# Kernel tuning notes

Measured on AMD Instinct MI355X. Metric: run time of the kernel, lower is better.

Reference implementation:

```python
import jax, jax.numpy as jnp
import numpy as np
import math

D_MODEL = 1024
RPN_D = 256
SUP_HW = 20  # support feature map is 20x20 -> 400 tokens


def _positional_encoding(max_len, d_model):
    pos = np.arange(max_len, dtype=np.float32)[:, None]
    div = np.exp(np.arange(0, d_model, 2, dtype=np.float32) * -(math.log(10000.0) / float(d_model)))
    pe = np.zeros((max_len, d_model), dtype=np.float32)
    pe[:, 0::2] = np.sin(pos * div)
    pe[:, 1::2] = np.cos(pos * div)
    return jnp.asarray(pe)


def setup_inputs() -> dict:
    key = jax.random.key(0)
    ks = jax.random.split(key, 6)
    B, S, H = 4, 5, 4
    fh, fw = 64, 64
    base_feat = jax.random.normal(ks[0], (B, D_MODEL, fh, fw), dtype=jnp.float32)
    support_feat = jax.random.normal(ks[1], (B, S, D_MODEL, SUP_HW, SUP_HW), dtype=jnp.float32)
    Qw = jax.random.normal(ks[2], (H, RPN_D, D_MODEL), dtype=jnp.float32) * 0.01
    Qb = jnp.zeros((H, RPN_D), dtype=jnp.float32)
    Kw = jax.random.normal(ks[3], (H, RPN_D, D_MODEL), dtype=jnp.float32) * 0.01
    Kb = jnp.zeros((H, RPN_D), dtype=jnp.float32)
    Mw = jax.random.normal(ks[4], (D_MODEL, H * D_MODEL), dtype=jnp.float32) * 0.02
    Mb = jnp.zeros((D_MODEL,), dtype=jnp.float32)
    return {"base_feat": base_feat, "support_feat": support_feat,
            "Qw": Qw, "Qb": Qb, "Kw": Kw, "Kb": Kb, "Mw": Mw, "Mb": Mb}


def reference(base_feat, support_feat, Qw, Qb, Kw, Kb, Mw, Mb):
    B, C, fh, fw = base_feat.shape
    S = support_feat.shape[1]
    H = Qw.shape[0]
    Lq = fh * fw
    Lk = SUP_HW * SUP_HW

    # support_mat: [S, B, Lk, C]  (transpose(0,1) then flatten spatial, then transpose)
    support_mat = jnp.transpose(support_feat, (1, 0, 2, 3, 4)).reshape(S, B, C, Lk)
    support_mat = jnp.transpose(support_mat, (0, 1, 3, 2))
    # query_mat: [B, Lq, C]
    query_mat = jnp.transpose(base_feat.reshape(B, C, Lq), (0, 2, 1))

    pe = _positional_encoding(400, D_MODEL)[:Lk]  # [Lk, C]
    s_mat = support_mat + pe[None, None]          # [S, B, Lk, C]

    # per-head projections (q is independent of shot, compute once)
    q = jnp.einsum('blc,hdc->hbld', query_mat, Qw) + Qb[:, None, None, :]   # [H,B,Lq,d]
    k = jnp.einsum('sbkc,hdc->hsbkd', s_mat, Kw) + Kb[:, None, None, None, :]  # [H,S,B,Lk,d]

    scores = jnp.einsum('hbld,hsbkd->hsblk', q, k) / math.sqrt(RPN_D)  # [H,S,B,Lq,Lk]
    attn = jax.nn.softmax(scores, axis=-1)
    z = jnp.einsum('hsblk,sbkc->hsblc', attn, s_mat)  # [H,S,B,Lq,C]

    # shot_mode == 'mean'
    z = jnp.mean(z, axis=1)  # [H,B,Lq,C]

    # concat heads along feature dim (head order preserved): [B,Lq,H*C]
    att = jnp.transpose(z, (1, 2, 0, 3)).reshape(B, Lq, H * C)
    att = jax.nn.relu(att @ Mw.T + Mb)  # [B,Lq,C]

    att = jnp.transpose(att, (0, 2, 1)).reshape(B, C, fh, fw)
    # attention_type == 'product'
    correlation_feat = base_feat * att
    return correlation_feat
```

## Files before the change

kernel.cpp:

```cpp
#include <hip/hip_runtime.h>
#include <stdint.h>

#define DEVI __device__ __forceinline__

typedef __attribute__((ext_vector_type(8))) short bf16x8;
typedef __attribute__((ext_vector_type(4))) float f32x4;
typedef __attribute__((ext_vector_type(4))) unsigned short us4;
typedef unsigned short u16;

constexpr int B_ = 4, S_ = 5, H_ = 4, C_ = 1024, D_ = 256;
constexpr int LQ = 4096, LK = 400, LKP = 448;

DEVI u16 f2b(float f){
  uint32_t x = __float_as_uint(f);
  uint32_t r = (x + 0x7FFFu + ((x >> 16) & 1u)) >> 16;
  return (u16)r;
}

typedef __attribute__((address_space(1))) const void ASG;
typedef __attribute__((address_space(3))) void ASL;
DEVI void gload16(const void* g, void* l){
  __builtin_amdgcn_global_load_lds((ASG*)g, (ASL*)l, 16, 0, 0);
}

__global__ __launch_bounds__(256) void k_cvt(const float* __restrict__ s, u16* __restrict__ d, int n4){
  int i = blockIdx.x*256 + threadIdx.x;
  if (i >= n4) return;
  float4 v = ((const float4*)s)[i];
  us4 o; o.x = f2b(v.x); o.y = f2b(v.y); o.z = f2b(v.z); o.w = f2b(v.w);
  *(us4*)(d + (size_t)i*4) = o;
}

__global__ __launch_bounds__(256) void k_transpose_x(const float* __restrict__ base, u16* __restrict__ Xb){
  __shared__ float t[32][33];
  int l0 = blockIdx.x*32, c0 = blockIdx.y*32, b = blockIdx.z;
  int tx = threadIdx.x & 31, ty = threadIdx.x >> 5;
  const float* src = base + ((size_t)b*C_ + c0)*LQ + l0;
  #pragma unroll
  for (int i=0;i<4;i++){ int cc = ty + i*8; t[cc][tx] = src[(size_t)cc*LQ + tx]; }
  __syncthreads();
  u16* dst = Xb + ((size_t)b*LQ + l0)*C_ + c0;
  #pragma unroll
  for (int i=0;i<4;i++){ int ll = ty + i*8; dst[(size_t)ll*C_ + tx] = f2b(t[tx][ll]); }
}

__global__ __launch_bounds__(256) void k_build_smat(const float* __restrict__ sup, u16* __restrict__ kc){
  __shared__ float t[32][33];
  int p0 = blockIdx.x*32, c0 = blockIdx.y*32;
  int s = blockIdx.z / B_, b = blockIdx.z % B_;
  int tx = threadIdx.x & 31, ty = threadIdx.x >> 5;
  const float* src = sup + ((size_t)(b*S_ + s)*C_ + c0)*LK + p0;
  #pragma unroll
  for (int i=0;i<4;i++){
    int cc = ty + i*8;
    int p = p0 + tx;
    int c = c0 + cc;
    float v = 0.f;
    if (p < LK){
      v = src[(size_t)cc*LK + tx];
      float dv = expf(-(float)(c & ~1) * (9.210340371976184f / 1024.f));
      float arg = (float)p * dv;
      v += (c & 1) ? cosf(arg) : sinf(arg);
    }
    t[cc][tx] = v;
  }
  __syncthreads();
  u16* dkc = kc + ((size_t)((s*B_ + b)*LKP + p0))*C_ + c0;
  #pragma unroll
  for (int i=0;i<4;i++){ int pp = ty + i*8; dkc[(size_t)pp*C_ + tx] = f2b(t[tx][pp]); }
}

DEVI void stage_half(const u16* P, int64_t ld, u16* dst, int wid, int r8, int s8){
  #pragma unroll
  for (int it=0; it<2; ++it){
    int ck = wid + it*8;
    gload16(P + (size_t)(ck*8 + r8)*ld + s8*8, dst + ck*512);
  }
}
DEVI bf16x8 ldsread(const u16* base, int row, int kk, int lane){
  int sl = ((kk<<2) + (lane>>4)) ^ (row & 7);
  return *(const bf16x8*)&base[row*64 + sl*8];
}

template<int CEPI, bool FIRST, bool FINAL, bool BIAS>
__global__ __launch_bounds__(512,1) void k8(
    const u16* __restrict__ A, const u16* __restrict__ Bm, void* __restrict__ Cm,
    const float* __restrict__ bias, const float* __restrict__ basep, const float* __restrict__ Mb,
    int tilesM, int64_t lda, int64_t ldb, int64_t ldc, int NT,
    int bdiv, int64_t aS0, int64_t aS1, int64_t bS0, int64_t bS1,
    int64_t cS0, int64_t cS1, int64_t aZ, int64_t bZ, int64_t cZ,
    int biasS0, float scale, int Nmax, int Mmax, int swz){
  __shared__ __align__(16) u16 lds[2][2][16384];
  int tid = threadIdx.x, lane = tid & 63, wid = tid >> 6;
  int bx = blockIdx.x;
  int mt, ntile;
  if (swz == 2){ int x = bx & 7, j = bx >> 3; mt = 2*x + (j >> 2); ntile = j & 3; }
  else {
    if (swz == 1) bx = (bx & 7) * (gridDim.x >> 3) + (bx >> 3);
    mt = bx % tilesM; ntile = bx / tilesM;
  }
  int z = blockIdx.y, i0 = z / bdiv, i1 = z % bdiv;
  int iz = blockIdx.z;
  const u16* Ab = A + i0*aS0 + i1*aS1 + iz*aZ + (size_t)mt*256*lda;
  const u16* Bb = Bm + i0*bS0 + i1*bS1 + iz*bZ + (size_t)ntile*256*ldb;
  int r8 = lane >> 3, s8 = (lane & 7) ^ r8;
  int wr = wid >> 2, wc = wid & 3;

  f32x4 acc[8][4];
  #pragma unroll
  for (int i=0;i<8;i++)
    #pragma unroll
    for (int j=0;j<4;j++) acc[i][j] = (f32x4){0.f,0.f,0.f,0.f};

  const u16 *ApS = Ab, *BpS = Bb;
  stage_half(ApS,                   lda, &lds[0][0][0],    wid, r8, s8);
  stage_half(ApS + (size_t)128*lda, lda, &lds[0][0][8192], wid, r8, s8);
  stage_half(BpS,                   ldb, &lds[0][1][0],    wid, r8, s8);
  stage_half(BpS + (size_t)128*ldb, ldb, &lds[0][1][8192], wid, r8, s8);
  ApS += 64; BpS += 64;

  for (int t = 0; t < NT; ++t){
    int cur = t & 1, nxt = cur ^ 1;
    bool pf = (t + 1 < NT);
    const u16* lA = &lds[cur][0][0];
    const u16* lB = &lds[cur][1][0];
    u16* sA = &lds[nxt][0][0];
    u16* sB = &lds[nxt][1][0];
    if (pf){
      stage_half(ApS,                   lda, sA,        wid, r8, s8);
      stage_half(ApS + (size_t)128*lda, lda, sA + 8192, wid, r8, s8);
      asm volatile("s_waitcnt vmcnt(4)" ::: "memory");
    } else {
      asm volatile("s_waitcnt vmcnt(0)" ::: "memory");
    }
    asm volatile("s_barrier" ::: "memory");

    bf16x8 bfr[4][2];
    #pragma unroll
    for (int jn=0;jn<4;jn++)
      #pragma unroll
      for (int kk=0;kk<2;kk++)
        bfr[jn][kk] = ldsread(lB, wc*64 + jn*16 + (lane & 15), kk, lane);

    #pragma unroll
    for (int p = 0; p < 4; ++p){
      bf16x8 af[2][2];
      #pragma unroll
      for (int dm=0;dm<2;dm++)
        #pragma unroll
        for (int kk=0;kk<2;kk++)
          af[dm][kk] = ldsread(lA, wr*128 + (p*2+dm)*16 + (lane & 15), kk, lane);
      __builtin_amdgcn_s_setprio(1);
      #pragma unroll
      for (int dm=0;dm<2;dm++)
        #pragma unroll
        for (int jn=0;jn<4;jn++)
          #pragma unroll
          for (int kk=0;kk<2;kk++)
            acc[p*2+dm][jn] = __builtin_amdgcn_mfma_f32_16x16x32_bf16(af[dm][kk], bfr[jn][kk], acc[p*2+dm][jn], 0,0,0);
      __builtin_amdgcn_s_setprio(0);
      if (p == 0 && pf) stage_half(BpS,                   ldb, sB,        wid, r8, s8);
      if (p == 1 && pf) stage_half(BpS + (size_t)128*ldb, ldb, sB + 8192, wid, r8, s8);
    }
    asm volatile("s_barrier" ::: "memory");
    if (pf){ ApS += 64; BpS += 64; }
  }

  int g = lane >> 4, c16 = lane & 15;
  if constexpr (CEPI == 0){
    u16* Cb = (u16*)Cm + i0*cS0 + i1*cS1 + iz*cZ;
    #pragma unroll
    for (int jn=0;jn<4;jn++){
      int n = ntile*256 + wc*64 + jn*16 + c16;
      if (n >= Nmax) continue;
      float bv = 0.f;
      if (BIAS) bv = bias[(size_t)i0*biasS0 + n];
      #pragma unroll
      for (int im=0;im<8;im++){
        int m = mt*256 + wr*128 + im*16 + g*4;
        if (m >= Mmax) continue;
        #pragma unroll
        for (int r=0;r<4;r++)
          Cb[(size_t)(m + r)*ldc + n] = f2b((acc[im][jn][r] + bv)*scale);
      }
    }
  } else {
    float* Cb = (float*)Cm + i0*cS0 + i1*cS1 + iz*cZ;
    const float* Bs = basep + i0*cS0 + i1*cS1 + iz*cZ;
    #pragma unroll
    for (int jn=0;jn<4;jn++){
      int n = ntile*256 + wc*64 + jn*16 + c16;
      float mbv = 0.f;
      if (FINAL) mbv = Mb[n];
      #pragma unroll
      for (int im=0;im<8;im++){
        int m = mt*256 + wr*128 + im*16 + g*4;
        float* p = Cb + (size_t)n*ldc + m;
        float4 v;
        v.x = acc[im][jn][0]; v.y = acc[im][jn][1]; v.z = acc[im][jn][2]; v.w = acc[im][jn][3];
        if (!FIRST){
          float4 old = *(const float4*)p;
          v.x += old.x; v.y += old.y; v.z += old.z; v.w += old.w;
        }
        if (FINAL){
          float4 bs = *(const float4*)(Bs + (size_t)n*ldc + m);
          v.x = bs.x * fmaxf(0.2f*v.x + mbv, 0.f);
          v.y = bs.y * fmaxf(0.2f*v.y + mbv, 0.f);
          v.z = bs.z * fmaxf(0.2f*v.z + mbv, 0.f);
          v.w = bs.w * fmaxf(0.2f*v.w + mbv, 0.f);
        }
        *(float4*)p = v;
      }
    }
  }
}

__global__ __launch_bounds__(512) void k_scores(
    const u16* __restrict__ qws, const u16* __restrict__ kws,
    u16* __restrict__ attn, int h0, int KVP, int padw, int nz){
  __shared__ __align__(16) u16 lQ[128*64];
  __shared__ __align__(16) u16 lK[400*64];
  int tid = threadIdx.x, lane = tid & 63, wid = tid >> 6;
  int m0 = blockIdx.x * 128;
  int b = blockIdx.y;
  int zz = blockIdx.z;
  int s = zz % 5, h = h0 + zz / 5;
  const u16* Qp = qws + ((size_t)(h*B_ + b)*LQ + m0)*D_;
  const u16* Kp = kws + ((size_t)((h*S_ + s)*B_ + b))*((size_t)LKP*D_);
  int r8 = lane >> 3, s8 = (lane & 7) ^ r8;
  f32x4 acc[25];
  #pragma unroll
  for (int t=0;t<25;t++) acc[t] = (f32x4){0.f,0.f,0.f,0.f};
  int wm = wid * 16;
  for (int k0 = 0; k0 < 256; k0 += 64){
    __syncthreads();
    #pragma unroll
    for (int c = 0; c < 2; ++c){
      int cc = wid + c*8;
      int row = cc*8 + r8;
      gload16(Qp + (size_t)row*D_ + k0 + s8*8, &lQ[cc*512]);
    }
    for (int cc = wid; cc < 50; cc += 8){
      int row = cc*8 + r8;
      gload16(Kp + (size_t)row*D_ + k0 + s8*8, &lK[cc*512]);
    }
    __syncthreads();
    #pragma unroll
    for (int kk = 0; kk < 2; ++kk){
      int rowA = wm + (lane & 15);
      int slA = ((kk<<2) + (lane>>4)) ^ (rowA & 7);
      bf16x8 af = *(const bf16x8*)&lQ[rowA*64 + slA*8];
      #pragma unroll
      for (int t=0;t<25;t++){
        int rowB = t*16 + (lane & 15);
        int slB = ((kk<<2) + (lane>>4)) ^ (rowB & 7);
        bf16x8 bf = *(const bf16x8*)&lK[rowB*64 + slB*8];
        acc[t] = __builtin_amdgcn_mfma_f32_16x16x32_bf16(af, bf, acc[t], 0,0,0);
      }
    }
  }
  float mx[4] = {-1e30f,-1e30f,-1e30f,-1e30f};
  #pragma unroll
  for (int t=0;t<25;t++)
    #pragma unroll
    for (int r=0;r<4;r++) mx[r] = fmaxf(mx[r], acc[t][r]);
  #pragma unroll
  for (int r=0;r<4;r++){
    mx[r] = fmaxf(mx[r], __shfl_xor(mx[r], 1));
    mx[r] = fmaxf(mx[r], __shfl_xor(mx[r], 2));
    mx[r] = fmaxf(mx[r], __shfl_xor(mx[r], 4));
    mx[r] = fmaxf(mx[r], __shfl_xor(mx[r], 8));
  }
  float sm[4] = {0.f,0.f,0.f,0.f};
  #pragma unroll
  for (int t=0;t<25;t++)
    #pragma unroll
    for (int r=0;r<4;r++){ float e = __expf(acc[t][r] - mx[r]); acc[t][r] = e; sm[r] += e; }
  #pragma unroll
  for (int r=0;r<4;r++){
    sm[r] += __shfl_xor(sm[r], 1);
    sm[r] += __shfl_xor(sm[r], 2);
    sm[r] += __shfl_xor(sm[r], 4);
    sm[r] += __shfl_xor(sm[r], 8);
    sm[r] = 1.f / sm[r];
  }
  u16* ap = attn + ((size_t)b*LQ + m0 + wm)*KVP + (size_t)zz*400;
  int g = lane >> 4, c16 = lane & 15;
  #pragma unroll
  for (int t=0;t<25;t++)
    #pragma unroll
    for (int r=0;r<4;r++)
      ap[(size_t)(g*4 + r)*KVP + t*16 + c16] = f2b(acc[t][r] * sm[r]);
  if (zz == nz - 1 && padw > 0){
    u16* base2 = attn + ((size_t)b*LQ + m0)*KVP + (KVP - padw);
    int total = 128 * padw;
    for (int i = tid; i < total; i += 512){
      int rr = i / padw, cc = i % padw;
      base2[(size_t)rr*KVP + cc] = 0;
    }
  }
}

extern "C" void kernel_launch(void* const* d_in, const int* in_sizes, int n_in,
                              void* d_out, int out_size, void* d_ws, size_t ws_size,
                              hipStream_t stream){
  const float* base = (const float*)d_in[0];
  const float* sup  = (const float*)d_in[1];
  const float* Qw   = (const float*)d_in[2];
  const float* Qb   = (const float*)d_in[3];
  const float* Kw   = (const float*)d_in[4];
  const float* Kb   = (const float*)d_in[5];
  const float* Mw   = (const float*)d_in[6];
  const float* Mb   = (const float*)d_in[7];
  float* out = (float*)d_out;
  char* ws = (char*)d_ws;

  const int GH = (ws_size >= 247988224ull) ? 2 : 1;
  const int NG = H_ / GH;
  const int NZ = GH * 5;
  const int KVP = (NZ*400 + 63) & ~63;
  const int NT = KVP / 64;
  const int PADW = KVP - NZ*400;

  u16* wQw = (u16*)(ws + 0);
  u16* wKw = (u16*)(ws + 2097152);
  u16* wMw = (u16*)(ws + 4194304);
  u16* wKC = (u16*)(ws + 12582912);
  u16* wK  = (u16*)(ws + 30932992);
  u16* wQ  = (u16*)(ws + 49283072);
  u16* wVt = (u16*)(ws + 82837504);
  u16* wAT = (u16*)(ws + 82837504 + (size_t)B_*C_*KVP*2);
  u16* wXb = wAT;

  const int BIG = 1 << 30;

  k_cvt<<<1024, 256, 0, stream>>>(Qw, wQw, 262144);
  k_cvt<<<1024, 256, 0, stream>>>(Kw, wKw, 262144);
  k_cvt<<<4096, 256, 0, stream>>>(Mw, wMw, 1048576);
  k_transpose_x<<<dim3(128, 32, 4), 256, 0, stream>>>(base, wXb);
  k_build_smat<<<dim3(14, 32, 20), 256, 0, stream>>>(sup, wKC);

  k8<0,false,false,true><<<dim3(2, 80, 1), 512, 0, stream>>>(
      wKC, wKw, wK, Kb, nullptr, nullptr,
      2, C_, C_, D_, 16,
      20, 0, (int64_t)LKP*C_, (int64_t)D_*C_, 0,
      (int64_t)S_*B_*LKP*D_, (int64_t)LKP*D_, 0, 0, 0,
      D_, 1.f, BIG, LKP, 0);

  k8<0,false,false,true><<<dim3(16, 16, 1), 512, 0, stream>>>(
      wXb, wQw, wQ, Qb, nullptr, nullptr,
      16, C_, C_, D_, 16,
      4, 0, (int64_t)LQ*C_, (int64_t)D_*C_, 0,
      (int64_t)B_*LQ*D_, (int64_t)LQ*D_, 0, 0, 0,
      D_, 1.f/16.f, BIG, BIG, 1);

  for (int g = 0; g < NG; ++g){
    k8<0,false,false,false><<<dim3(8, NZ, 4), 512, 0, stream>>>(
        wMw + (size_t)(g*GH)*C_, wKC, wVt, nullptr, nullptr, nullptr,
        4, (int64_t)H_*C_, C_, KVP, 16,
        5, (int64_t)C_, 0, 0, (int64_t)B_*LKP*C_,
        2000, 400, 0, (int64_t)LKP*C_, (int64_t)C_*KVP,
        0, 1.f, 400, BIG, 0);

    k_scores<<<dim3(32, 4, NZ), 512, 0, stream>>>(wQ, wK, wAT, g*GH, KVP, PADW, NZ);

    if (g == 0 && NG > 1){
      k8<1,true,false,false><<<dim3(64, 4, 1), 512, 0, stream>>>(
          wAT, wVt, out, nullptr, base, Mb,
          16, KVP, KVP, LQ, NT,
          1, (int64_t)LQ*KVP, 0, (int64_t)C_*KVP, 0,
          (int64_t)C_*LQ, 0, 0, 0, 0,
          0, 1.f, BIG, BIG, 2);
    } else if (g == NG - 1){
      k8<1,false,true,false><<<dim3(64, 4, 1), 512, 0, stream>>>(
          wAT, wVt, out, nullptr, base, Mb,
          16, KVP, KVP, LQ, NT,
          1, (int64_t)LQ*KVP, 0, (int64_t)C_*KVP, 0,
          (int64_t)C_*LQ, 0, 0, 0, 0,
          0, 1.f, BIG, BIG, 2);
    } else {
      k8<1,false,false,false><<<dim3(64, 4, 1), 512, 0, stream>>>(
          wAT, wVt, out, nullptr, base, Mb,
          16, KVP, KVP, LQ, NT,
          1, (int64_t)LQ*KVP, 0, (int64_t)C_*KVP, 0,
          (int64_t)C_*LQ, 0, 0, 0, 0,
          0, 1.f, BIG, BIG, 2);
    }
  }
}
```

Before: 701.8 us.

## Retile score kernel as 2x4 wave grid with cross-wave softmax reduction

The score kernel now splits the 128x400 tile across waves as two row groups times four key-column groups, with each wave computing a 64x112 sub-tile. The old layout had each wave take 16 rows across all 25 key tiles. Each LDS K fragment is now reused across four A fragments, cutting LDS reads per MFMA. Because each row is now spread over four waves, softmax max and sum need a shared-memory reduction with extra barriers. The K load is unrolled and padded to 448 rows, and MFMA issue priority is raised with setprio.

```diff
diff --git a/kernel.cpp b/kernel.cpp
--- a/kernel.cpp
+++ b/kernel.cpp
@@ -215,11 +215,13 @@
   }
 }
 
-__global__ __launch_bounds__(512) void k_scores(
+__global__ __launch_bounds__(512,1) void k_scores(
     const u16* __restrict__ qws, const u16* __restrict__ kws,
     u16* __restrict__ attn, int h0, int KVP, int padw, int nz){
   __shared__ __align__(16) u16 lQ[128*64];
-  __shared__ __align__(16) u16 lK[400*64];
+  __shared__ __align__(16) u16 lK[448*64];
+  __shared__ float red[128][4];
+  __shared__ float rowv[128];
   int tid = threadIdx.x, lane = tid & 63, wid = tid >> 6;
   int m0 = blockIdx.x * 128;
   int b = blockIdx.y;
@@ -228,69 +230,166 @@
   const u16* Qp = qws + ((size_t)(h*B_ + b)*LQ + m0)*D_;
   const u16* Kp = kws + ((size_t)((h*S_ + s)*B_ + b))*((size_t)LKP*D_);
   int r8 = lane >> 3, s8 = (lane & 7) ^ r8;
-  f32x4 acc[25];
-  #pragma unroll
-  for (int t=0;t<25;t++) acc[t] = (f32x4){0.f,0.f,0.f,0.f};
-  int wm = wid * 16;
+  int c16 = lane & 15, g = lane >> 4;
+  int wm2 = wid >> 2, wkv = wid & 3;
+
+  f32x4 acc[4][7];
+  #pragma unroll
+  for (int m=0;m<4;m++)
+    #pragma unroll
+    for (int tt=0;tt<7;tt++) acc[m][tt] = (f32x4){0.f,0.f,0.f,0.f};
+
   for (int k0 = 0; k0 < 256; k0 += 64){
     __syncthreads();
     #pragma unroll
     for (int c = 0; c < 2; ++c){
       int cc = wid + c*8;
-      int row = cc*8 + r8;
-      gload16(Qp + (size_t)row*D_ + k0 + s8*8, &lQ[cc*512]);
-    }
-    for (int cc = wid; cc < 50; cc += 8){
-      int row = cc*8 + r8;
-      gload16(Kp + (size_t)row*D_ + k0 + s8*8, &lK[cc*512]);
+      gload16(Qp + (size_t)(cc*8 + r8)*D_ + k0 + s8*8, &lQ[cc*512]);
+    }
+    #pragma unroll
+    for (int i = 0; i < 7; ++i){
+      int ck = wid + i*8;
+      gload16(Kp + (size_t)(ck*8 + r8)*D_ + k0 + s8*8, &lK[ck*512]);
     }
     __syncthreads();
-    #pragma unroll
-    for (int kk = 0; kk < 2; ++kk){
-      int rowA = wm + (lane & 15);
-      int slA = ((kk<<2) + (lane>>4)) ^ (rowA & 7);
-      bf16x8 af = *(const bf16x8*)&lQ[rowA*64 + slA*8];
-      #pragma unroll
-      for (int t=0;t<25;t++){
-        int rowB = t*16 + (lane & 15);
-        int slB = ((kk<<2) + (lane>>4)) ^ (rowB & 7);
-        bf16x8 bf = *(const bf16x8*)&lK[rowB*64 + slB*8];
-        acc[t] = __builtin_amdgcn_mfma_f32_16x16x32_bf16(af, bf, acc[t], 0,0,0);
-      }
-    }
-  }
-  float mx[4] = {-1e30f,-1e30f,-1e30f,-1e30f};
-  #pragma unroll
-  for (int t=0;t<25;t++)
-    #pragma unroll
-    for (int r=0;r<4;r++) mx[r] = fmaxf(mx[r], acc[t][r]);
-  #pragma unroll
-  for (int r=0;r<4;r++){
-    mx[r] = fmaxf(mx[r], __shfl_xor(mx[r], 1));
-    mx[r] = fmaxf(mx[r], __shfl_xor(mx[r], 2));
-    mx[r] = fmaxf(mx[r], __shfl_xor(mx[r], 4));
-    mx[r] = fmaxf(mx[r], __shfl_xor(mx[r], 8));
-  }
-  float sm[4] = {0.f,0.f,0.f,0.f};
-  #pragma unroll
-  for (int t=0;t<25;t++)
-    #pragma unroll
-    for (int r=0;r<4;r++){ float e = __expf(acc[t][r] - mx[r]); acc[t][r] = e; sm[r] += e; }
-  #pragma unroll
-  for (int r=0;r<4;r++){
-    sm[r] += __shfl_xor(sm[r], 1);
-    sm[r] += __shfl_xor(sm[r], 2);
-    sm[r] += __shfl_xor(sm[r], 4);
-    sm[r] += __shfl_xor(sm[r], 8);
-    sm[r] = 1.f / sm[r];
-  }
-  u16* ap = attn + ((size_t)b*LQ + m0 + wm)*KVP + (size_t)zz*400;
-  int g = lane >> 4, c16 = lane & 15;
-  #pragma unroll
-  for (int t=0;t<25;t++)
-    #pragma unroll
-    for (int r=0;r<4;r++)
-      ap[(size_t)(g*4 + r)*KVP + t*16 + c16] = f2b(acc[t][r] * sm[r]);
+
+    bf16x8 af[4][2];
+    #pragma unroll
+    for (int m=0;m<4;m++)
+      #pragma unroll
+      for (int kk=0;kk<2;kk++)
+        af[m][kk] = ldsread(lQ, wm2*64 + m*16 + c16, kk, lane);
+    __builtin_amdgcn_s_setprio(1);
+    #pragma unroll
+    for (int tt=0;tt<7;tt++)
+      #pragma unroll
+      for (int kk=0;kk<2;kk++){
+        bf16x8 bf = ldsread(lK, wkv*112 + tt*16 + c16, kk, lane);
+        #pragma unroll
+        for (int m=0;m<4;m++)
+          acc[m][tt] = __builtin_amdgcn_mfma_f32_16x16x32_bf16(af[m][kk], bf, acc[m][tt], 0,0,0);
+      }
+    __builtin_amdgcn_s_setprio(0);
+  }
+
+  float pmax[4][4];
+  if (wkv == 3){
+    #pragma unroll
+    for (int m=0;m<4;m++)
+      #pragma unroll
+      for (int r=0;r<4;r++){
+        float v = acc[m][0][r];
+        v = fmaxf(v, acc[m][1][r]); v = fmaxf(v, acc[m][2][r]); v = fmaxf(v, acc[m][3][r]);
+        pmax[m][r] = v;
+      }
+  } else {
+    #pragma unroll
+    for (int m=0;m<4;m++)
+      #pragma unroll
+      for (int r=0;r<4;r++){
+        float v = acc[m][0][r];
+        v = fmaxf(v, acc[m][1][r]); v = fmaxf(v, acc[m][2][r]); v = fmaxf(v, acc[m][3][r]);
+        v = fmaxf(v, acc[m][4][r]); v = fmaxf(v, acc[m][5][r]); v = fmaxf(v, acc[m][6][r]);
+        pmax[m][r] = v;
+      }
+  }
+  #pragma unroll
+  for (int m=0;m<4;m++)
+    #pragma unroll
+    for (int r=0;r<4;r++){
+      pmax[m][r] = fmaxf(pmax[m][r], __shfl_xor(pmax[m][r], 1));
+      pmax[m][r] = fmaxf(pmax[m][r], __shfl_xor(pmax[m][r], 2));
+      pmax[m][r] = fmaxf(pmax[m][r], __shfl_xor(pmax[m][r], 4));
+      pmax[m][r] = fmaxf(pmax[m][r], __shfl_xor(pmax[m][r], 8));
+    }
+  if (c16 == 0){
+    #pragma unroll
+    for (int m=0;m<4;m++)
+      #pragma unroll
+      for (int r=0;r<4;r++)
+        red[wm2*64 + m*16 + g*4 + r][wkv] = pmax[m][r];
+  }
+  __syncthreads();
+  if (tid < 128)
+    rowv[tid] = fmaxf(fmaxf(red[tid][0], red[tid][1]), fmaxf(red[tid][2], red[tid][3]));
+  __syncthreads();
+  float mxr[4][4];
+  #pragma unroll
+  for (int m=0;m<4;m++)
+    #pragma unroll
+    for (int r=0;r<4;r++) mxr[m][r] = rowv[wm2*64 + m*16 + g*4 + r];
+
+  float ps[4][4];
+  #pragma unroll
+  for (int m=0;m<4;m++)
+    #pragma unroll
+    for (int r=0;r<4;r++) ps[m][r] = 0.f;
+  if (wkv == 3){
+    #pragma unroll
+    for (int tt=0;tt<4;tt++)
+      #pragma unroll
+      for (int m=0;m<4;m++)
+        #pragma unroll
+        for (int r=0;r<4;r++){
+          float e = __expf(acc[m][tt][r] - mxr[m][r]);
+          acc[m][tt][r] = e; ps[m][r] += e;
+        }
+  } else {
+    #pragma unroll
+    for (int tt=0;tt<7;tt++)
+      #pragma unroll
+      for (int m=0;m<4;m++)
+        #pragma unroll
+        for (int r=0;r<4;r++){
+          float e = __expf(acc[m][tt][r] - mxr[m][r]);
+          acc[m][tt][r] = e; ps[m][r] += e;
+        }
+  }
+  #pragma unroll
+  for (int m=0;m<4;m++)
+    #pragma unroll
+    for (int r=0;r<4;r++){
+      ps[m][r] += __shfl_xor(ps[m][r], 1);
+      ps[m][r] += __shfl_xor(ps[m][r], 2);
+      ps[m][r] += __shfl_xor(ps[m][r], 4);
+      ps[m][r] += __shfl_xor(ps[m][r], 8);
+    }
+  if (c16 == 0){
+    #pragma unroll
+    for (int m=0;m<4;m++)
+      #pragma unroll
+      for (int r=0;r<4;r++)
+        red[wm2*64 + m*16 + g*4 + r][wkv] = ps[m][r];
+  }
+  __syncthreads();
+  if (tid < 128)
+    rowv[tid] = 1.f / (red[tid][0] + red[tid][1] + red[tid][2] + red[tid][3]);
+  __syncthreads();
+
+  u16* ap = attn + ((size_t)b*LQ + m0)*KVP + (size_t)zz*400;
+  if (wkv == 3){
+    #pragma unroll
+    for (int m=0;m<4;m++)
+      #pragma unroll
+      for (int r=0;r<4;r++){
+        int rowl = wm2*64 + m*16 + g*4 + r;
+        float rs = rowv[rowl];
+        #pragma unroll
+        for (int tt=0;tt<4;tt++)
+          ap[(size_t)rowl*KVP + wkv*112 + tt*16 + c16] = f2b(acc[m][tt][r] * rs);
+      }
+  } else {
+    #pragma unroll
+    for (int m=0;m<4;m++)
+      #pragma unroll
+      for (int r=0;r<4;r++){
+        int rowl = wm2*64 + m*16 + g*4 + r;
+        float rs = rowv[rowl];
+        #pragma unroll
+        for (int tt=0;tt<7;tt++)
+          ap[(size_t)rowl*KVP + wkv*112 + tt*16 + c16] = f2b(acc[m][tt][r] * rs);
+      }
+  }
   if (zz == nz - 1 && padw > 0){
     u16* base2 = attn + ((size_t)b*LQ + m0)*KVP + (KVP - padw);
     int total = 128 * padw;
```

Result: slower. 728.5 us (+3.8%).

## Replace attention-value GEMM with ping-pong pipelined k8p kernel

Applied to the files above, without the earlier changes.

Adds a dedicated k8p kernel for the attn×V GEMM. It swaps the operand roles, putting V rows on M and queries on N. It double-buffers LDS and splits each K step into four phases, interleaving global→LDS staging with MFMA work under barriers and setprio. The aim is to hide load latency behind the matrix ops in the largest GEMM. In exchange, the epilogue now writes scalar, transposed-orientation stores instead of float4, which can cost coalescing.

```diff
diff --git a/kernel.cpp b/kernel.cpp
--- a/kernel.cpp
+++ b/kernel.cpp
@@ -215,6 +215,136 @@
   }
 }
 
+#define K8P_PHASE(LA, LB, P, READB, STAGE, VM)                                         \
+  {                                                                                    \
+    if (READB){                                                                        \
+      _Pragma("unroll")                                                                \
+      for (int jn=0;jn<4;jn++)                                                         \
+        _Pragma("unroll")                                                              \
+        for (int kk=0;kk<2;kk++)                                                       \
+          bfr[jn][kk] = ldsread((LB), wc*64 + jn*16 + c16, kk, lane);                  \
+    }                                                                                  \
+    bf16x8 af[2][2];                                                                   \
+    _Pragma("unroll")                                                                  \
+    for (int dm=0;dm<2;dm++)                                                           \
+      _Pragma("unroll")                                                                \
+      for (int kk=0;kk<2;kk++)                                                         \
+        af[dm][kk] = ldsread((LA), wr*128 + ((P)*2+dm)*16 + c16, kk, lane);            \
+    STAGE;                                                                             \
+    VM;                                                                                \
+    asm volatile("s_barrier" ::: "memory");                                            \
+    __builtin_amdgcn_s_setprio(1);                                                     \
+    _Pragma("unroll")                                                                  \
+    for (int dm=0;dm<2;dm++)                                                           \
+      _Pragma("unroll")                                                                \
+      for (int jn=0;jn<4;jn++)                                                         \
+        _Pragma("unroll")                                                              \
+        for (int kk=0;kk<2;kk++)                                                       \
+          acc[(P)*2+dm][jn] = __builtin_amdgcn_mfma_f32_16x16x32_bf16(af[dm][kk], bfr[jn][kk], acc[(P)*2+dm][jn], 0,0,0); \
+    __builtin_amdgcn_s_setprio(0);                                                     \
+    asm volatile("s_barrier" ::: "memory");                                            \
+  }
+
+template<bool FIRST, bool FINAL>
+__global__ __launch_bounds__(512,1) void k8p(
+    const u16* __restrict__ A, const u16* __restrict__ Bm, float* __restrict__ Cm,
+    const float* __restrict__ basep, const float* __restrict__ Mb,
+    int KVP, int NT){
+  __shared__ __align__(16) u16 lds[2][2][16384];
+  int tid = threadIdx.x, lane = tid & 63, wid = tid >> 6;
+  int bx = blockIdx.x;
+  int x = bx & 7, j = bx >> 3;
+  int ntile = x*2 + (j >> 2);
+  int mt = j & 3;
+  int b = blockIdx.y;
+  const u16* Ab = A + ((size_t)b*C_ + (size_t)mt*256)*KVP;
+  const u16* Bb = Bm + ((size_t)b*LQ + (size_t)ntile*256)*KVP;
+  int64_t lda = KVP, ldb = KVP;
+  int r8 = lane >> 3, s8 = (lane & 7) ^ r8;
+  int c16 = lane & 15, g = lane >> 4;
+  int wr = wid >> 2, wc = wid & 3;
+
+  f32x4 acc[8][4];
+  #pragma unroll
+  for (int i=0;i<8;i++)
+    #pragma unroll
+    for (int jn=0;jn<4;jn++) acc[i][jn] = (f32x4){0.f,0.f,0.f,0.f};
+  bf16x8 bfr[4][2];
+
+  stage_half(Bb,                   ldb, &lds[0][1][0],    wid, r8, s8);
+  stage_half(Bb + (size_t)128*ldb, ldb, &lds[0][1][8192], wid, r8, s8);
+  stage_half(Ab,                   lda, &lds[0][0][0],    wid, r8, s8);
+  stage_half(Ab + (size_t)128*lda, lda, &lds[0][0][8192], wid, r8, s8);
+  stage_half(Bb + 64,                   ldb, &lds[1][1][0],    wid, r8, s8);
+  stage_half(Bb + (size_t)128*ldb + 64, ldb, &lds[1][1][8192], wid, r8, s8);
+  asm volatile("s_waitcnt vmcnt(4)" ::: "memory");
+  asm volatile("s_barrier" ::: "memory");
+
+  const u16* lA0 = &lds[0][0][0]; const u16* lB0 = &lds[0][1][0];
+  const u16* lA1 = &lds[1][0][0]; const u16* lB1 = &lds[1][1][0];
+
+  int nPairs = NT >> 1;
+  for (int i = 0; i < nPairs; ++i){
+    int u = 2*i;
+    bool s2 = (u + 2 < NT), s3 = (u + 3 < NT);
+    K8P_PHASE(lA0, lB0, 0, true,
+      { stage_half(Ab + (size_t)(u+1)*64,                     lda, &lds[1][0][0],    wid, r8, s8);
+        stage_half(Ab + (size_t)128*lda + (size_t)(u+1)*64,   lda, &lds[1][0][8192], wid, r8, s8); },
+      {});
+    K8P_PHASE(lA0, lB0, 1, false,
+      { if (s2) stage_half(Bb + (size_t)(u+2)*64,             ldb, &lds[0][1][0],    wid, r8, s8); },
+      {});
+    K8P_PHASE(lA0, lB0, 2, false,
+      { if (s2) stage_half(Bb + (size_t)128*ldb + (size_t)(u+2)*64, ldb, &lds[0][1][8192], wid, r8, s8); },
+      {});
+    K8P_PHASE(lA0, lB0, 3, false, {},
+      { if (s2) { asm volatile("s_waitcnt vmcnt(4)" ::: "memory"); }
+        else    { asm volatile("s_waitcnt vmcnt(0)" ::: "memory"); } });
+    K8P_PHASE(lA1, lB1, 0, true,
+      { if (s2) stage_half(Ab + (size_t)(u+2)*64,             lda, &lds[0][0][0],    wid, r8, s8); },
+      {});
+    K8P_PHASE(lA1, lB1, 1, false,
+      { if (s2) stage_half(Ab + (size_t)128*lda + (size_t)(u+2)*64, lda, &lds[0][0][8192], wid, r8, s8); },
+      {});
+    K8P_PHASE(lA1, lB1, 2, false,
+      { if (s3) stage_half(Bb + (size_t)(u+3)*64,             ldb, &lds[1][1][0],    wid, r8, s8); },
+      {});
+    K8P_PHASE(lA1, lB1, 3, false,
+      { if (s3) stage_half(Bb + (size_t)128*ldb + (size_t)(u+3)*64, ldb, &lds[1][1][8192], wid, r8, s8); },
+      { if (s3) { asm volatile("s_waitcnt vmcnt(4)" ::: "memory"); }
+        else    { asm volatile("s_waitcnt vmcnt(0)" ::: "memory"); } });
+  }
+  if (NT & 1){
+    K8P_PHASE(lA0, lB0, 0, true,  {}, {});
+    K8P_PHASE(lA0, lB0, 1, false, {}, {});
+    K8P_PHASE(lA0, lB0, 2, false, {}, {});
+    K8P_PHASE(lA0, lB0, 3, false, {}, {});
+  }
+
+  float* Cb = Cm + (size_t)b*C_*LQ;
+  const float* Bs = basep + (size_t)b*C_*LQ;
+  #pragma unroll
+  for (int jn=0;jn<4;jn++){
+    int n = ntile*256 + wc*64 + jn*16 + c16;
+    #pragma unroll
+    for (int im=0;im<8;im++){
+      int m0 = mt*256 + wr*128 + im*16 + g*4;
+      #pragma unroll
+      for (int r=0;r<4;r++){
+        int m = m0 + r;
+        float v = acc[im][jn][r];
+        float* p = Cb + (size_t)m*LQ + n;
+        if (!FIRST) v += *p;
+        if (FINAL){
+          float bs = Bs[(size_t)m*LQ + n];
+          v = bs * fmaxf(0.2f*v + Mb[m], 0.f);
+        }
+        *p = v;
+      }
+    }
+  }
+}
+
 __global__ __launch_bounds__(512) void k_scores(
     const u16* __restrict__ qws, const u16* __restrict__ kws,
     u16* __restrict__ attn, int h0, int KVP, int padw, int nz){
@@ -365,26 +495,11 @@
     k_scores<<<dim3(32, 4, NZ), 512, 0, stream>>>(wQ, wK, wAT, g*GH, KVP, PADW, NZ);
 
     if (g == 0 && NG > 1){
-      k8<1,true,false,false><<<dim3(64, 4, 1), 512, 0, stream>>>(
-          wAT, wVt, out, nullptr, base, Mb,
-          16, KVP, KVP, LQ, NT,
-          1, (int64_t)LQ*KVP, 0, (int64_t)C_*KVP, 0,
-          (int64_t)C_*LQ, 0, 0, 0, 0,
-          0, 1.f, BIG, BIG, 2);
+      k8p<true,false><<<dim3(64, 4), 512, 0, stream>>>(wVt, wAT, out, base, Mb, KVP, NT);
     } else if (g == NG - 1){
-      k8<1,false,true,false><<<dim3(64, 4, 1), 512, 0, stream>>>(
-          wAT, wVt, out, nullptr, base, Mb,
-          16, KVP, KVP, LQ, NT,
-          1, (int64_t)LQ*KVP, 0, (int64_t)C_*KVP, 0,
-          (int64_t)C_*LQ, 0, 0, 0, 0,
-          0, 1.f, BIG, BIG, 2);
+      k8p<false,true><<<dim3(64, 4), 512, 0, stream>>>(wVt, wAT, out, base, Mb, KVP, NT);
     } else {
-      k8<1,false,false,false><<<dim3(64, 4, 1), 512, 0, stream>>>(
-          wAT, wVt, out, nullptr, base, Mb,
-          16, KVP, KVP, LQ, NT,
-          1, (int64_t)LQ*KVP, 0, (int64_t)C_*KVP, 0,
-          (int64_t)C_*LQ, 0, 0, 0, 0,
-          0, 1.f, BIG, BIG, 2);
-    }
-  }
-}
+      k8p<false,false><<<dim3(64, 4), 512, 0, stream>>>(wVt, wAT, out, base, Mb, KVP, NT);
+    }
+  }
+}
```

Result: slower. 783.3 us (+11.6%).
